# Kernel tuning notes

Measured on AMD Instinct MI355X. Metric: run time of the kernel, lower is better.

## Reference

```python
import jax, jax.numpy as jnp
import numpy as np

N_FFT = 1024
HOP = 256
WIN_LEN = N_FFT  # win_length == n_fft
PAD = (WIN_LEN - HOP) // 2  # 'same' padding


def hann_window(n):
    # torch.hann_window default (periodic=True): 0.5*(1-cos(2*pi*k/n))
    k = jnp.arange(n, dtype=jnp.float32)
    return 0.5 * (1.0 - jnp.cos(2.0 * jnp.pi * k / n))


def setup_inputs() -> dict:
    key = jax.random.key(0)
    k1, k2 = jax.random.split(key)
    B, L, D = 8, 2048, 512
    x = jax.random.normal(k1, (B, L, D), dtype=jnp.float32)
    W = jax.random.normal(k2, (D, N_FFT + 2), dtype=jnp.float32) * (1.0 / np.sqrt(D))
    b = jnp.zeros((N_FFT + 2,), dtype=jnp.float32)
    return {"x": x, "W": W, "b": b}


def reference(x, W, b):
    # Linear projection: (B, L, n_fft+2)
    h = jnp.einsum("bld,do->blo", x, W) + b
    nbins = N_FFT // 2 + 1  # 513
    mag = jnp.minimum(jnp.exp(h[..., :nbins]), 100.0)  # exp + clip max=100
    p = h[..., nbins:]
    # Complex STFT coefficients S: (B, L, nbins)
    S = mag * (jnp.cos(p) + 1j * jnp.sin(p))
    # Per-frame inverse rFFT (norm='backward' = default): (B, L, n_fft)
    frames = jnp.fft.irfft(S, n=N_FFT, axis=-1)
    win = hann_window(WIN_LEN)
    frames = frames * win  # windowed frames
    B, T = frames.shape[0], frames.shape[1]
    out_size = (T - 1) * HOP + WIN_LEN
    # Overlap-add via scatter-add
    idx = jnp.arange(T)[:, None] * HOP + jnp.arange(WIN_LEN)[None, :]  # (T, n_fft)
    y = jnp.zeros((B, out_size), dtype=frames.dtype).at[:, idx].add(frames)
    env = jnp.zeros((out_size,), dtype=frames.dtype).at[idx].add(
        jnp.broadcast_to(win * win, (T, WIN_LEN))
    )
    y = y[:, PAD:-PAD] / env[PAD:-PAD]
    return y
```

## Files before the change

### kernel.cpp

```cpp
#include <hip/hip_runtime.h>
#include <math.h>


using half8 = __attribute__((ext_vector_type(8))) _Float16;
using f32x4 = __attribute__((ext_vector_type(4))) float;

#define TWO_PI_OVER_1024 0.006135923151542565f

#define OFF_A2 0
#define OFF_B2 35651584UL
#define OFF_A1 37879808UL
#define OFF_B1 54657024UL
#define OFF_FR 37879808UL

__device__ __forceinline__ float hannf(int s) {
    return 0.5f * (1.0f - cosf(TWO_PI_OVER_1024 * (float)s));
}

__device__ __forceinline__ void stage16(const void* g, void* lds) {
    __builtin_amdgcn_global_load_lds(
        (const __attribute__((address_space(1))) void*)g,
        (__attribute__((address_space(3))) void*)lds,
        16, 0, 0);
}


__global__ __launch_bounds__(256)
void conv_x_k(const float* __restrict__ x, _Float16* __restrict__ A1)
{
    const size_t tid = (size_t)blockIdx.x * 256 + threadIdx.x;
    const int l   = (int)(tid & 63);
    const size_t f = tid >> 6;
    const int mts = (int)(f & 7);
    const size_t g = f >> 3;
    const int kt  = (int)(g & 15);
    const int mtb = (int)(g >> 4);
    const int m   = mtb * 128 + mts * 16 + (l & 15);
    const int k0  = kt * 32 + (l >> 4) * 8;
    const float* xp = x + (size_t)m * 512 + k0;
    const float4 v0 = *(const float4*)xp;
    const float4 v1 = *(const float4*)(xp + 4);
    const float vv[8] = {v0.x, v0.y, v0.z, v0.w, v1.x, v1.y, v1.z, v1.w};
    half8 o;
#pragma unroll
    for (int j = 0; j < 8; ++j) o[j] = (_Float16)vv[j];
    *(half8*)(A1 + tid * 8) = o;
}

__global__ __launch_bounds__(256)
void prep_k(const float* __restrict__ W, _Float16* __restrict__ B1,
            _Float16* __restrict__ B2)
{
    if (blockIdx.x < 288) {
        const int tid = blockIdx.x * 256 + threadIdx.x;
        const int l  = tid & 63;
        const int f  = tid >> 6;
        const int t8 = f & 7;
        const int g  = f >> 3;
        const int kt = g & 15;
        const int bx = g >> 4;
        const int side = t8 >> 2;
        const int nt   = t8 & 3;
        const int c    = bx * 64 + nt * 16 + (l & 15);
        const int k0   = kt * 32 + (l >> 4) * 8;
        const int wcol = side ? (513 + c) : c;
        half8 o;
#pragma unroll
        for (int j = 0; j < 8; ++j) {
            float v = (c < 513) ? W[(size_t)(k0 + j) * 1026 + wcol] : 0.0f;
            o[j] = (_Float16)v;
        }
        *(half8*)(B1 + (size_t)tid * 8) = o;
    } else {
        const int tid = (blockIdx.x - 288) * 256 + threadIdx.x;
        const int l  = tid & 63;
        const int f  = tid >> 6;
        const int nt = f % 6;
        const int g  = f / 6;
        const int kt = g % 34;
        const int nblk = g / 34;
        const int n  = nblk * 96 + nt * 16 + (l & 15);
        const int kk0 = kt * 32 + (l >> 4) * 8;
        const float win = hannf(n) * (1.0f / 1024.0f);
        half8 o;
#pragma unroll
        for (int j = 0; j < 8; ++j) {
            const int kk = kk0 + j;
            float v = 0.0f;
            if (kk < 544) {
                const int k = kk;
                if (k < 513) {
                    const float coef = (k == 0 || k == 512) ? 1.0f : 2.0f;
                    v = coef * cosf(TWO_PI_OVER_1024 * (float)((k * n) & 1023)) * win;
                }
            } else {
                const int k = kk - 544;
                if (k < 513) {
                    const float coef = (k == 0 || k == 512) ? 1.0f : 2.0f;
                    v = -coef * sinf(TWO_PI_OVER_1024 * (float)((k * n) & 1023)) * win;
                }
            }
            o[j] = (_Float16)v;
        }
        *(half8*)(B2 + (size_t)tid * 8) = o;
    }
}


__device__ __forceinline__ void store_a2(_Float16* __restrict__ A2, int m, int k, float v)
{
    const int mt2 = m >> 4, mr = m & 15;
    const int kt2 = k >> 5, kc = k & 31;
    const int l2 = (kc >> 3) * 16 + mr;
    const int j2 = kc & 7;
    const int mtb = mt2 >> 3, mts = mt2 & 7;
    const size_t idx = ((((size_t)mtb * 34 + kt2) * 8 + mts) * 64 + l2) * 8 + j2;
    A2[idx] = (_Float16)v;
}

__global__ __launch_bounds__(256, 3)
void gemm1_k(const _Float16* __restrict__ A, const _Float16* __restrict__ B,
             const float* __restrict__ bias, _Float16* __restrict__ A2)
{
    __shared__ _Float16 Ash[2][8 * 512];
    __shared__ _Float16 Bsh[2][8 * 512];
    const int t = threadIdx.x, w = t >> 6, l = t & 63;

    const int lin = blockIdx.x;
    const int xcd = lin & 7, slot = lin >> 3;
    const int mblk = xcd * 16 + slot / 9;
    const int bx   = slot % 9;

    const int wm = (w & 1) * 4;
    const int q  = w >> 1;
    const int jt[4] = {2 * q, 2 * q + 1, 4 + 2 * q, 5 + 2 * q};

    f32x4 acc[4][4];
#pragma unroll
    for (int i = 0; i < 4; ++i)
#pragma unroll
        for (int j = 0; j < 4; ++j) acc[i][j] = (f32x4)0.0f;

    const int lane8 = l * 8;
    const _Float16* Ab = A + ((size_t)mblk * 16 * 8) * 512 + lane8;
    const _Float16* Bb = B + ((size_t)bx * 16 * 8) * 512 + lane8;

    for (int step = 0; step < 8; ++step) {
        const int kt0 = 2 * step;
        __syncthreads();
#pragma unroll
        for (int i = 0; i < 4; ++i) {
            const int s = 4 * w + i;
            const int u = s >> 3, r = s & 7;
            stage16(Ab + ((size_t)(kt0 + u) * 8 + r) * 512, &Ash[u][r * 512]);
            stage16(Bb + ((size_t)(kt0 + u) * 8 + r) * 512, &Bsh[u][r * 512]);
        }
        __syncthreads();

#pragma unroll
        for (int u = 0; u < 2; ++u) {
            half8 a[4], b[4];
#pragma unroll
            for (int i = 0; i < 4; ++i)
                a[i] = *(const half8*)&Ash[u][(wm + i) * 512 + lane8];
#pragma unroll
            for (int j = 0; j < 4; ++j)
                b[j] = *(const half8*)&Bsh[u][jt[j] * 512 + lane8];
#pragma unroll
            for (int i = 0; i < 4; ++i)
#pragma unroll
                for (int j = 0; j < 4; ++j)
                    acc[i][j] = __builtin_amdgcn_mfma_f32_16x16x32_f16(a[i], b[j], acc[i][j], 0, 0, 0);
        }
    }

    const int r4 = (l >> 4) * 4, c16 = l & 15;
#pragma unroll
    for (int i = 0; i < 4; ++i) {
        const int mbase = mblk * 128 + (wm + i) * 16 + r4;
#pragma unroll
        for (int p = 0; p < 2; ++p) {
            const int c = bx * 64 + (2 * q + p) * 16 + c16;
            const bool valid = (c < 513);
            const float bm = valid ? bias[c] : 0.0f;
            const float bp = valid ? bias[513 + c] : 0.0f;
#pragma unroll
            for (int r = 0; r < 4; ++r) {
                float Sr = 0.0f, Si = 0.0f;
                if (valid) {
                    const float mag = fminf(expf(acc[i][p][r] + bm), 100.0f);
                    const float ph  = acc[i][2 + p][r] + bp;
                    Sr = mag * cosf(ph);
                    Si = mag * sinf(ph);
                }
                if (c < 544) {
                    store_a2(A2, mbase + r, c, Sr);
                    store_a2(A2, mbase + r, 544 + c, Si);
                }
            }
        }
    }
}


__device__ __forceinline__ void mma43(const _Float16* __restrict__ As,
                                      const _Float16* __restrict__ Bs,
                                      int wm, int wn, int lane16, f32x4 (&acc)[4][3])
{
    half8 a[4], b[3];
#pragma unroll
    for (int i = 0; i < 4; ++i) a[i] = *(const half8*)&As[(wm + i) * 512 + lane16];
#pragma unroll
    for (int j = 0; j < 3; ++j) b[j] = *(const half8*)&Bs[(wn + j) * 512 + lane16];
#pragma unroll
    for (int i = 0; i < 4; ++i)
#pragma unroll
        for (int j = 0; j < 3; ++j)
            acc[i][j] = __builtin_amdgcn_mfma_f32_16x16x32_f16(a[i], b[j], acc[i][j], 0, 0, 0);
}

__global__ __launch_bounds__(256, 3)
void gemm2_k(const _Float16* __restrict__ A, const _Float16* __restrict__ Bas,
             _Float16* __restrict__ C)
{
    __shared__ _Float16 As[2][8 * 512];
    __shared__ _Float16 Bs[2][6 * 512];
    const int t = threadIdx.x, w = t >> 6, l = t & 63;

    const int lin = blockIdx.x;
    const int xcd = lin & 7, slot = lin >> 3;
    const int mblk = xcd * 16 + slot / 6;
    const int nblk = slot % 6;

    const int wm = (w & 1) * 4, wn = (w >> 1) * 3;

    f32x4 accC[4][3], accD[4][3];
#pragma unroll
    for (int i = 0; i < 4; ++i)
#pragma unroll
        for (int j = 0; j < 3; ++j) { accC[i][j] = (f32x4)0.0f; accD[i][j] = (f32x4)0.0f; }

    const int lane16 = l * 8;

    for (int step = 0; step < 17; ++step) {
        const int kt0 = 2 * step;
        __syncthreads();
#pragma unroll
        for (int i = 0; i < 4; ++i) {
            const int ta = 4 * w + i;
            const int u = ta >> 3, mts = ta & 7;
            const _Float16* Ag = A + ((((size_t)mblk * 34 + (kt0 + u)) * 8 + mts) * 512) + lane16;
            stage16(Ag, &As[u][mts * 512]);
        }
#pragma unroll
        for (int i = 0; i < 3; ++i) {
            const int tb = 3 * w + i;
            const int u = tb / 6, nt = tb % 6;
            const _Float16* Bg = Bas + ((((size_t)nblk * 34 + (kt0 + u)) * 6 + nt) * 512) + lane16;
            stage16(Bg, &Bs[u][nt * 512]);
        }
        __syncthreads();

#pragma unroll
        for (int u = 0; u < 2; ++u) {
            const int kt = kt0 + u;
            if (kt < 17) mma43(As[u], Bs[u], wm, wn, lane16, accC);
            else         mma43(As[u], Bs[u], wm, wn, lane16, accD);
        }
    }

    const int r4 = (l >> 4) * 4, c0 = l & 15;
#pragma unroll
    for (int i = 0; i < 4; ++i) {
        const int m = mblk * 128 + (wm + i) * 16 + r4;
#pragma unroll
        for (int j = 0; j < 3; ++j) {
            const int n = nblk * 96 + (wn + j) * 16 + c0;
#pragma unroll
            for (int r = 0; r < 4; ++r) {
                const float cv = accC[i][j][r];
                const float dv = accD[i][j][r];
                _Float16* row = C + (size_t)(m + r) * 1024;
                if (n < 513)           row[n]        = (_Float16)(cv + dv);
                if (n >= 1 && n < 512) row[1024 - n] = (_Float16)(cv - dv);
            }
        }
    }
}


__global__ __launch_bounds__(256)
void ola_kernel(const _Float16* __restrict__ frames, float* __restrict__ out)
{
    const int idx = blockIdx.x * 256 + threadIdx.x;
    const int b = idx >> 19;
    const int j = idx & 524287;
    const int n = j + 384;

    int t_hi = n >> 8;
    if (t_hi > 2047) t_hi = 2047;
    const int t_lo = (n >= 1023) ? ((n - 1023 + 255) >> 8) : 0;

    float acc = 0.0f, env = 0.0f;
    for (int tt = t_lo; tt <= t_hi; ++tt) {
        const int s = n - (tt << 8);
        const float wv = hannf(s);
        acc += (float)frames[(((size_t)(b * 2048 + tt)) << 10) + s];
        env += wv * wv;
    }
    out[idx] = acc / env;
}


extern "C" void kernel_launch(void* const* d_in, const int* in_sizes, int n_in,
                              void* d_out, int out_size, void* d_ws, size_t ws_size,
                              hipStream_t stream)
{
    const float* x = (const float*)d_in[0];
    const float* W = (const float*)d_in[1];
    const float* b = (const float*)d_in[2];
    float* out = (float*)d_out;
    char* ws = (char*)d_ws;

    _Float16* A2 = (_Float16*)(ws + OFF_A2);
    _Float16* B2 = (_Float16*)(ws + OFF_B2);
    _Float16* A1 = (_Float16*)(ws + OFF_A1);
    _Float16* B1 = (_Float16*)(ws + OFF_B1);
    _Float16* frames = (_Float16*)(ws + OFF_FR);

    conv_x_k<<<4096, 256, 0, stream>>>(x, A1);
    prep_k<<<594, 256, 0, stream>>>(W, B1, B2);

    gemm1_k<<<1152, 256, 0, stream>>>(A1, B1, b, A2);
    gemm2_k<<<768, 256, 0, stream>>>(A2, B2, frames);

    ola_kernel<<<out_size / 256, 256, 0, stream>>>(frames, out);
}
```

Baseline: 194.8 us.

## Merge input conversion into prep kernel, use fast trig intrinsics, raise gemm1 occupancy

Folds the x-to-fp16 conversion kernel into the weight/DFT-basis prep kernel so one launch does all three jobs. It also swaps cosf/sinf/expf for the __cosf/__sinf/__expf intrinsics in the DFT basis, the window and the gemm1 epilogue. Separately, gemm1's launch_bounds minimum block count goes from 3 to 4. The aims are less launch overhead, a cheaper transcendental epilogue and more resident waves, at the cost of lower accuracy for phase arguments outside a small range and possible register spills in gemm1.

```diff
diff --git a/kernel.cpp b/kernel.cpp
--- a/kernel.cpp
+++ b/kernel.cpp
@@ -14,7 +14,7 @@
 #define OFF_FR 37879808UL
 
 __device__ __forceinline__ float hannf(int s) {
-    return 0.5f * (1.0f - cosf(TWO_PI_OVER_1024 * (float)s));
+    return 0.5f * (1.0f - __cosf(TWO_PI_OVER_1024 * (float)s));
 }
 
 __device__ __forceinline__ void stage16(const void* g, void* lds) {
@@ -24,35 +24,32 @@
         16, 0, 0);
 }
 
-
 __global__ __launch_bounds__(256)
-void conv_x_k(const float* __restrict__ x, _Float16* __restrict__ A1)
-{
-    const size_t tid = (size_t)blockIdx.x * 256 + threadIdx.x;
-    const int l   = (int)(tid & 63);
-    const size_t f = tid >> 6;
-    const int mts = (int)(f & 7);
-    const size_t g = f >> 3;
-    const int kt  = (int)(g & 15);
-    const int mtb = (int)(g >> 4);
-    const int m   = mtb * 128 + mts * 16 + (l & 15);
-    const int k0  = kt * 32 + (l >> 4) * 8;
-    const float* xp = x + (size_t)m * 512 + k0;
-    const float4 v0 = *(const float4*)xp;
-    const float4 v1 = *(const float4*)(xp + 4);
-    const float vv[8] = {v0.x, v0.y, v0.z, v0.w, v1.x, v1.y, v1.z, v1.w};
-    half8 o;
-#pragma unroll
-    for (int j = 0; j < 8; ++j) o[j] = (_Float16)vv[j];
-    *(half8*)(A1 + tid * 8) = o;
-}
-
-__global__ __launch_bounds__(256)
-void prep_k(const float* __restrict__ W, _Float16* __restrict__ B1,
+void prep_k(const float* __restrict__ x, const float* __restrict__ W,
+            _Float16* __restrict__ A1, _Float16* __restrict__ B1,
             _Float16* __restrict__ B2)
 {
-    if (blockIdx.x < 288) {
-        const int tid = blockIdx.x * 256 + threadIdx.x;
+    const int bid = blockIdx.x;
+    if (bid < 4096) {
+        const size_t tid = (size_t)bid * 256 + threadIdx.x;
+        const int l   = (int)(tid & 63);
+        const size_t f = tid >> 6;
+        const int mts = (int)(f & 7);
+        const size_t g = f >> 3;
+        const int kt  = (int)(g & 15);
+        const int mtb = (int)(g >> 4);
+        const int m   = mtb * 128 + mts * 16 + (l & 15);
+        const int k0  = kt * 32 + (l >> 4) * 8;
+        const float* xp = x + (size_t)m * 512 + k0;
+        const float4 v0 = *(const float4*)xp;
+        const float4 v1 = *(const float4*)(xp + 4);
+        const float vv[8] = {v0.x, v0.y, v0.z, v0.w, v1.x, v1.y, v1.z, v1.w};
+        half8 o;
+#pragma unroll
+        for (int j = 0; j < 8; ++j) o[j] = (_Float16)vv[j];
+        *(half8*)(A1 + tid * 8) = o;
+    } else if (bid < 4384) {
+        const int tid = (bid - 4096) * 256 + threadIdx.x;
         const int l  = tid & 63;
         const int f  = tid >> 6;
         const int t8 = f & 7;
@@ -72,7 +69,7 @@
         }
         *(half8*)(B1 + (size_t)tid * 8) = o;
     } else {
-        const int tid = (blockIdx.x - 288) * 256 + threadIdx.x;
+        const int tid = (bid - 4384) * 256 + threadIdx.x;
         const int l  = tid & 63;
         const int f  = tid >> 6;
         const int nt = f % 6;
@@ -91,13 +88,13 @@
                 const int k = kk;
                 if (k < 513) {
                     const float coef = (k == 0 || k == 512) ? 1.0f : 2.0f;
-                    v = coef * cosf(TWO_PI_OVER_1024 * (float)((k * n) & 1023)) * win;
+                    v = coef * __cosf(TWO_PI_OVER_1024 * (float)((k * n) & 1023)) * win;
                 }
             } else {
                 const int k = kk - 544;
                 if (k < 513) {
                     const float coef = (k == 0 || k == 512) ? 1.0f : 2.0f;
-                    v = -coef * sinf(TWO_PI_OVER_1024 * (float)((k * n) & 1023)) * win;
+                    v = -coef * __sinf(TWO_PI_OVER_1024 * (float)((k * n) & 1023)) * win;
                 }
             }
             o[j] = (_Float16)v;
@@ -118,7 +115,7 @@
     A2[idx] = (_Float16)v;
 }
 
-__global__ __launch_bounds__(256, 3)
+__global__ __launch_bounds__(256, 4)
 void gemm1_k(const _Float16* __restrict__ A, const _Float16* __restrict__ B,
              const float* __restrict__ bias, _Float16* __restrict__ A2)
 {
@@ -188,10 +185,10 @@
             for (int r = 0; r < 4; ++r) {
                 float Sr = 0.0f, Si = 0.0f;
                 if (valid) {
-                    const float mag = fminf(expf(acc[i][p][r] + bm), 100.0f);
+                    const float mag = fminf(__expf(acc[i][p][r] + bm), 100.0f);
                     const float ph  = acc[i][2 + p][r] + bp;
-                    Sr = mag * cosf(ph);
-                    Si = mag * sinf(ph);
+                    Sr = mag * __cosf(ph);
+                    Si = mag * __sinf(ph);
                 }
                 if (c < 544) {
                     store_a2(A2, mbase + r, c, Sr);
@@ -328,8 +325,7 @@
     _Float16* B1 = (_Float16*)(ws + OFF_B1);
     _Float16* frames = (_Float16*)(ws + OFF_FR);
 
-    conv_x_k<<<4096, 256, 0, stream>>>(x, A1);
-    prep_k<<<594, 256, 0, stream>>>(W, B1, B2);
+    prep_k<<<4690, 256, 0, stream>>>(x, W, A1, B1, B2);
 
     gemm1_k<<<1152, 256, 0, stream>>>(A1, B1, b, A2);
     gemm2_k<<<768, 256, 0, stream>>>(A2, B2, frames);
```

Measured after the change: 167.2 us. -14.2%, faster.
